# Performance work log

Hardware: AMD Instinct MI355X
Metric: run time of the kernel (lower is better)

Reference implementation:

```python
import jax, jax.numpy as jnp
import numpy as np

N, E, G = 50000, 800000, 64
IN_DIM, HID, HEADS = 8, 64, 4
HC = HID * HEADS  # 256
EPS = 1e-5


def _gatv2(h, src, dst, ea, wl, bl, wr, br, we, att, bias):
    # h: [N, F_in]; ea: [E, 1]; att: [HEADS, HID]
    xl = (h @ wl + bl).reshape(N, HEADS, HID)        # source transform
    xr = (h @ wr + br).reshape(N, HEADS, HID)        # target transform
    ee = (ea @ we).reshape(E, HEADS, HID)            # edge embedding (no bias)
    m = xl[src] + xr[dst] + ee                       # [E, H, C]
    m = jax.nn.leaky_relu(m, 0.2)
    logits = jnp.einsum('ehc,hc->eh', m, att)        # [E, H]
    # softmax over incoming edges of each target node
    mx = jax.ops.segment_max(logits, dst, num_segments=N)
    ex = jnp.exp(logits - mx[dst])
    den = jax.ops.segment_sum(ex, dst, num_segments=N)
    alpha = ex / den[dst]                            # [E, H]
    out = jax.ops.segment_sum(xl[src] * alpha[..., None], dst, num_segments=N)
    return out.reshape(N, HC) + bias


def setup_inputs() -> dict:
    key = jax.random.key(0)
    ks = jax.random.split(key, 32)
    s = lambda fan: 1.0 / np.sqrt(fan)
    d = {}
    d['x'] = jax.random.normal(ks[0], (N, IN_DIM), jnp.float32)
    d['edge_attr'] = jax.random.normal(ks[1], (E, 1), jnp.float32)
    d['edge_index'] = jax.random.randint(ks[2], (2, E), 0, N, jnp.int64)
    d['batch'] = jnp.sort(jax.random.randint(ks[3], (N,), 0, G, jnp.int64))
    d['enc_w'] = jax.random.normal(ks[4], (IN_DIM, HID), jnp.float32) * s(IN_DIM)
    d['enc_b'] = jnp.zeros((HID,), jnp.float32)
    # gat1: in = HID
    d['g1_wl'] = jax.random.normal(ks[5], (HID, HC), jnp.float32) * s(HID)
    d['g1_bl'] = jnp.zeros((HC,), jnp.float32)
    d['g1_wr'] = jax.random.normal(ks[6], (HID, HC), jnp.float32) * s(HID)
    d['g1_br'] = jnp.zeros((HC,), jnp.float32)
    d['g1_we'] = jax.random.normal(ks[7], (1, HC), jnp.float32)
    d['g1_att'] = jax.random.normal(ks[8], (HEADS, HID), jnp.float32) * s(HID)
    d['g1_bias'] = jnp.zeros((HC,), jnp.float32)
    # gat2: in = HC
    d['g2_wl'] = jax.random.normal(ks[9], (HC, HC), jnp.float32) * s(HC)
    d['g2_bl'] = jnp.zeros((HC,), jnp.float32)
    d['g2_wr'] = jax.random.normal(ks[10], (HC, HC), jnp.float32) * s(HC)
    d['g2_br'] = jnp.zeros((HC,), jnp.float32)
    d['g2_we'] = jax.random.normal(ks[11], (1, HC), jnp.float32)
    d['g2_att'] = jax.random.normal(ks[12], (HEADS, HID), jnp.float32) * s(HID)
    d['g2_bias'] = jnp.zeros((HC,), jnp.float32)
    # post MLP + head
    d['p1_w'] = jax.random.normal(ks[13], (HC, 128), jnp.float32) * s(HC)
    d['p1_b'] = jnp.zeros((128,), jnp.float32)
    d['ln_g'] = jnp.ones((128,), jnp.float32)
    d['ln_b'] = jnp.zeros((128,), jnp.float32)
    d['p2_w'] = jax.random.normal(ks[14], (128, HID), jnp.float32) * s(128)
    d['p2_b'] = jnp.zeros((HID,), jnp.float32)
    d['head_w'] = jax.random.normal(ks[15], (HID, 1), jnp.float32) * s(HID)
    d['head_b'] = jnp.zeros((1,), jnp.float32)
    return d


def reference(x, edge_attr, edge_index, batch, enc_w, enc_b,
              g1_wl, g1_bl, g1_wr, g1_br, g1_we, g1_att, g1_bias,
              g2_wl, g2_bl, g2_wr, g2_br, g2_we, g2_att, g2_bias,
              p1_w, p1_b, ln_g, ln_b, p2_w, p2_b, head_w, head_b):
    src, dst = edge_index[0], edge_index[1]
    h = jax.nn.relu(x @ enc_w + enc_b)
    h = jax.nn.relu(_gatv2(h, src, dst, edge_attr, g1_wl, g1_bl, g1_wr, g1_br, g1_we, g1_att, g1_bias))
    h = jax.nn.relu(_gatv2(h, src, dst, edge_attr, g2_wl, g2_bl, g2_wr, g2_br, g2_we, g2_att, g2_bias))
    # global mean pool over graphs
    counts = jax.ops.segment_sum(jnp.ones((N,), h.dtype), batch, num_segments=G)
    g = jax.ops.segment_sum(h, batch, num_segments=G) / jnp.maximum(counts, 1.0)[:, None]
    # post MLP: Linear -> LayerNorm -> ReLU -> (dropout=eval noop) -> Linear -> ReLU
    z = g @ p1_w + p1_b
    mu = jnp.mean(z, axis=-1, keepdims=True)
    var = jnp.var(z, axis=-1, keepdims=True)
    z = (z - mu) * jax.lax.rsqrt(var + EPS) * ln_g + ln_b
    z = jax.nn.relu(z)
    z = jax.nn.relu(z @ p2_w + p2_b)
    return (z @ head_w + head_b)[:, 0]
```

## Files before the change

### kernel.cpp

```cpp
#include <hip/hip_runtime.h>
#include <hip/hip_bf16.h>
#include <math.h>

#define N_NODES 50000
#define N_EDGES 800000
#define N_GRAPHS 64
#define HCD 256
#define HIDD 64


__global__ void zero_i32(int* __restrict__ p, int n) {
  int i = blockIdx.x * blockDim.x + threadIdx.x;
  if (i < n) p[i] = 0;
}

__global__ void hist_kernel(const int* __restrict__ dst, int* __restrict__ counts, int ne) {
  int i = blockIdx.x * blockDim.x + threadIdx.x;
  if (i < ne) atomicAdd(&counts[dst[i]], 1);
}

__global__ __launch_bounds__(256) void scan1_kernel(const int* __restrict__ counts,
                                                    int* __restrict__ offs,
                                                    int* __restrict__ bsum, int n) {
  int t = threadIdx.x, lane = t & 63, w = t >> 6;
  int i = blockIdx.x * 256 + t;
  int v = (i < n) ? counts[i] : 0;
  int x = v;
  #pragma unroll
  for (int off = 1; off < 64; off <<= 1) {
    int tmp = __shfl_up(x, off);
    if (lane >= off) x += tmp;
  }
  __shared__ int wsum[4], woff[4];
  if (lane == 63) wsum[w] = x;
  __syncthreads();
  if (t == 0) {
    int s = 0;
    #pragma unroll
    for (int k = 0; k < 4; ++k) { woff[k] = s; s += wsum[k]; }
    bsum[blockIdx.x] = s;
  }
  __syncthreads();
  if (i < n) offs[i] = woff[w] + x - v;
}

__global__ __launch_bounds__(256) void scan2_kernel(int* __restrict__ bsum, int nblk) {
  int t = threadIdx.x, lane = t & 63, w = t >> 6;
  int v = (t < nblk) ? bsum[t] : 0;
  int x = v;
  #pragma unroll
  for (int off = 1; off < 64; off <<= 1) {
    int tmp = __shfl_up(x, off);
    if (lane >= off) x += tmp;
  }
  __shared__ int wsum[4], woff[4];
  if (lane == 63) wsum[w] = x;
  __syncthreads();
  if (t == 0) {
    int s = 0;
    #pragma unroll
    for (int k = 0; k < 4; ++k) { woff[k] = s; s += wsum[k]; }
  }
  __syncthreads();
  if (t < nblk) bsum[t] = woff[w] + x - v;
}

__global__ void scan3_kernel(int* __restrict__ offs, const int* __restrict__ bsum,
                             int* __restrict__ cursor, int n) {
  int i = blockIdx.x * blockDim.x + threadIdx.x;
  if (i < n) {
    int v = offs[i] + bsum[i >> 8];
    offs[i] = v;
    cursor[i] = v;
  } else if (i == n) {
    offs[n] = N_EDGES;
  }
}

__global__ void scatter_kernel(const int* __restrict__ src, const int* __restrict__ dst,
                               const float* __restrict__ ea, int* __restrict__ cursor,
                               int* __restrict__ ssrc, float* __restrict__ sea, int ne) {
  int i = blockIdx.x * blockDim.x + threadIdx.x;
  if (i < ne) {
    int d = dst[i];
    int pos = atomicAdd(&cursor[d], 1);
    ssrc[pos] = src[i];
    sea[pos] = ea[i];
  }
}


__global__ void encoder_kernel(const float* __restrict__ x, const float* __restrict__ w,
                               const float* __restrict__ b, float* __restrict__ h0, int n_nodes) {
  int idx = blockIdx.x * blockDim.x + threadIdx.x;
  if (idx >= n_nodes * HIDD) return;
  int n = idx >> 6, c = idx & 63;
  float acc = b[c];
  #pragma unroll
  for (int k = 0; k < 8; ++k) acc += x[n * 8 + k] * w[k * 64 + c];
  h0[idx] = fmaxf(acc, 0.f);
}


template<int K>
__global__ __launch_bounds__(256) void transform_kernel(
    const float* __restrict__ h,
    const float* __restrict__ wl, const float* __restrict__ bl,
    const float* __restrict__ wr, const float* __restrict__ br,
    float* __restrict__ xl, float* __restrict__ xr, int n_nodes)
{
  constexpr int NT = 32;
  __shared__ float hs[NT * K];
  int n0 = blockIdx.x * NT;
  const float* __restrict__ w   = blockIdx.y ? wr : wl;
  const float* __restrict__ bb  = blockIdx.y ? br : bl;
  float* __restrict__ outp      = blockIdx.y ? xr : xl;

  for (int idx4 = threadIdx.x; idx4 < NT * K / 4; idx4 += 256) {
    int i = idx4 / (K / 4), kq = idx4 - i * (K / 4);
    int n = n0 + i;
    float4 v = make_float4(0.f, 0.f, 0.f, 0.f);
    if (n < n_nodes) v = *(const float4*)&h[n * K + 4 * kq];
    *(float4*)&hs[i * K + 4 * kq] = v;
  }
  __syncthreads();

  const int cx = threadIdx.x & 63;
  const int ny = threadIdx.x >> 6;
  float acc[8][4];
  #pragma unroll
  for (int i = 0; i < 8; ++i)
    #pragma unroll
    for (int j = 0; j < 4; ++j) acc[i][j] = 0.f;

  const float* hrow = &hs[(ny * 8) * K];
  float4 wc = *(const float4*)&w[4 * cx];
  for (int k = 0; k < K; ++k) {
    float4 wn = wc;
    if (k + 1 < K) wn = *(const float4*)&w[(k + 1) * 256 + 4 * cx];
    #pragma unroll
    for (int i = 0; i < 8; ++i) {
      float hv = hrow[i * K + k];
      acc[i][0] = fmaf(hv, wc.x, acc[i][0]);
      acc[i][1] = fmaf(hv, wc.y, acc[i][1]);
      acc[i][2] = fmaf(hv, wc.z, acc[i][2]);
      acc[i][3] = fmaf(hv, wc.w, acc[i][3]);
    }
    wc = wn;
  }

  float4 b4 = *(const float4*)&bb[4 * cx];
  #pragma unroll
  for (int i = 0; i < 8; ++i) {
    int n = n0 + ny * 8 + i;
    if (n < n_nodes) {
      float4 o;
      o.x = acc[i][0] + b4.x; o.y = acc[i][1] + b4.y;
      o.z = acc[i][2] + b4.z; o.w = acc[i][3] + b4.w;
      *(float4*)&outp[n * 256 + 4 * cx] = o;
    }
  }
}


__global__ __launch_bounds__(256) void gat_aggregate_kernel(
    const float* __restrict__ xl, const float* __restrict__ xr,
    const int* __restrict__ offs, const int* __restrict__ ssrc,
    const float* __restrict__ sea,
    const float* __restrict__ we, const float* __restrict__ att,
    const float* __restrict__ bias, float* __restrict__ out, int n_nodes)
{
  int n = blockIdx.x;
  if (n >= n_nodes) return;
  int t = threadIdx.x, lane = t & 63, wv = t >> 6;
  const float4 xr4 = *(const float4*)&xr[n * HCD + 4 * lane];
  const float4 we4 = *(const float4*)&we[4 * lane];
  const float4 at4 = *(const float4*)&att[4 * lane];
  int beg = offs[n], end = offs[n + 1];
  float runmax = -INFINITY, den = 0.f;
  float4 acc = make_float4(0.f, 0.f, 0.f, 0.f);

  int j = beg + wv;
  int s = (j < end) ? ssrc[j] : 0;
  float eav = (j < end) ? sea[j] : 0.f;
  while (j < end) {
    int jn = j + 4;
    int s2 = 0; float ea2 = 0.f;
    if (jn < end) { s2 = ssrc[jn]; ea2 = sea[jn]; }
    float4 xlv = *(const float4*)&xl[s * HCD + 4 * lane];
    float4 m;
    m.x = xlv.x + fmaf(eav, we4.x, xr4.x);
    m.y = xlv.y + fmaf(eav, we4.y, xr4.y);
    m.z = xlv.z + fmaf(eav, we4.z, xr4.z);
    m.w = xlv.w + fmaf(eav, we4.w, xr4.w);
    m.x = (m.x > 0.f) ? m.x : 0.2f * m.x;
    m.y = (m.y > 0.f) ? m.y : 0.2f * m.y;
    m.z = (m.z > 0.f) ? m.z : 0.2f * m.z;
    m.w = (m.w > 0.f) ? m.w : 0.2f * m.w;
    float p = fmaf(m.w, at4.w, fmaf(m.z, at4.z, fmaf(m.y, at4.y, m.x * at4.x)));
    #pragma unroll
    for (int off = 1; off < 16; off <<= 1) p += __shfl_xor(p, off);
    float nm = fmaxf(runmax, p);
    float sc = __expf(runmax - nm);
    float wgt = __expf(p - nm);
    den = fmaf(den, sc, wgt);
    acc.x = fmaf(acc.x, sc, wgt * xlv.x);
    acc.y = fmaf(acc.y, sc, wgt * xlv.y);
    acc.z = fmaf(acc.z, sc, wgt * xlv.z);
    acc.w = fmaf(acc.w, sc, wgt * xlv.w);
    runmax = nm;
    s = s2; eav = ea2; j = jn;
  }

  __shared__ float smax[4][64], sden[4][64];
  __shared__ float4 sacc[4][64];
  smax[wv][lane] = runmax; sden[wv][lane] = den; sacc[wv][lane] = acc;
  __syncthreads();
  if (wv == 0) {
    float m0 = smax[0][lane], m1 = smax[1][lane], m2 = smax[2][lane], m3 = smax[3][lane];
    float M = fmaxf(fmaxf(m0, m1), fmaxf(m2, m3));
    float4 a = make_float4(0.f, 0.f, 0.f, 0.f);
    if (M > -INFINITY) {
      float s0 = __expf(m0 - M), s1 = __expf(m1 - M), s2 = __expf(m2 - M), s3 = __expf(m3 - M);
      float d = sden[0][lane] * s0 + sden[1][lane] * s1 + sden[2][lane] * s2 + sden[3][lane] * s3;
      float4 a0 = sacc[0][lane], a1 = sacc[1][lane], a2 = sacc[2][lane], a3 = sacc[3][lane];
      a.x = a0.x * s0 + a1.x * s1 + a2.x * s2 + a3.x * s3;
      a.y = a0.y * s0 + a1.y * s1 + a2.y * s2 + a3.y * s3;
      a.z = a0.z * s0 + a1.z * s1 + a2.z * s2 + a3.z * s3;
      a.w = a0.w * s0 + a1.w * s1 + a2.w * s2 + a3.w * s3;
      float inv = 1.f / d;
      a.x *= inv; a.y *= inv; a.z *= inv; a.w *= inv;
    }
    float4 b4 = *(const float4*)&bias[4 * lane];
    float4 o;
    o.x = fmaxf(a.x + b4.x, 0.f);
    o.y = fmaxf(a.y + b4.y, 0.f);
    o.z = fmaxf(a.z + b4.z, 0.f);
    o.w = fmaxf(a.w + b4.w, 0.f);
    *(float4*)&out[n * HCD + 4 * lane] = o;
  }
}


__device__ __forceinline__ int lbound(const int* __restrict__ a, int n, int key) {
  int lo = 0, hi = n;
  while (lo < hi) { int mid = (lo + hi) >> 1; if (a[mid] < key) lo = mid + 1; else hi = mid; }
  return lo;
}

__global__ __launch_bounds__(256) void pool_kernel(const float* __restrict__ h,
                                                   const int* __restrict__ batch,
                                                   float* __restrict__ gmean) {
  int g = blockIdx.x;
  int t = threadIdx.x, lane = t & 63, wv = t >> 6;
  __shared__ int sb, se;
  if (t == 0) {
    sb = lbound(batch, N_NODES, g);
    se = lbound(batch, N_NODES, g + 1);
  }
  __syncthreads();
  int beg = sb, end = se;
  float4 acc = make_float4(0.f, 0.f, 0.f, 0.f);
  for (int n = beg + wv; n < end; n += 4) {
    float4 v = *(const float4*)&h[n * HCD + 4 * lane];
    acc.x += v.x; acc.y += v.y; acc.z += v.z; acc.w += v.w;
  }
  __shared__ float4 sacc[4][64];
  sacc[wv][lane] = acc;
  __syncthreads();
  if (wv == 0) {
    float4 a0 = sacc[0][lane], a1 = sacc[1][lane], a2 = sacc[2][lane], a3 = sacc[3][lane];
    float cnt = (float)((end - beg) > 1 ? (end - beg) : 1);
    float inv = 1.f / cnt;
    float4 o;
    o.x = (a0.x + a1.x + a2.x + a3.x) * inv;
    o.y = (a0.y + a1.y + a2.y + a3.y) * inv;
    o.z = (a0.z + a1.z + a2.z + a3.z) * inv;
    o.w = (a0.w + a1.w + a2.w + a3.w) * inv;
    *(float4*)&gmean[g * HCD + 4 * lane] = o;
  }
}


__global__ __launch_bounds__(128) void mlp_kernel(
    const float* __restrict__ gmean,
    const float* __restrict__ p1_w, const float* __restrict__ p1_b,
    const float* __restrict__ ln_g, const float* __restrict__ ln_b,
    const float* __restrict__ p2_w, const float* __restrict__ p2_b,
    const float* __restrict__ head_w, const float* __restrict__ head_b,
    float* __restrict__ out)
{
  int g = blockIdx.x, t = threadIdx.x;
  __shared__ float gv[256];
  __shared__ float zs[128];
  __shared__ float z2s[64];
  __shared__ float sums[2][2];
  gv[t] = gmean[g * 256 + t];
  gv[t + 128] = gmean[g * 256 + 128 + t];
  __syncthreads();
  float acc = p1_b[t];
  for (int k = 0; k < 256; ++k) acc += gv[k] * p1_w[k * 128 + t];
  float s1 = acc, s2 = acc * acc;
  #pragma unroll
  for (int off = 32; off >= 1; off >>= 1) {
    s1 += __shfl_xor(s1, off);
    s2 += __shfl_xor(s2, off);
  }
  int wid = t >> 6, lane = t & 63;
  if (lane == 0) { sums[wid][0] = s1; sums[wid][1] = s2; }
  __syncthreads();
  float S1 = sums[0][0] + sums[1][0];
  float S2 = sums[0][1] + sums[1][1];
  float mu = S1 * (1.f / 128.f);
  float var = S2 * (1.f / 128.f) - mu * mu;
  float rstd = rsqrtf(var + 1e-5f);
  float z = (acc - mu) * rstd * ln_g[t] + ln_b[t];
  zs[t] = fmaxf(z, 0.f);
  __syncthreads();
  if (t < 64) {
    float a2 = p2_b[t];
    for (int k = 0; k < 128; ++k) a2 += zs[k] * p2_w[k * 64 + t];
    z2s[t] = fmaxf(a2, 0.f);
  }
  __syncthreads();
  if (t < 64) {
    float p = z2s[t] * head_w[t];
    #pragma unroll
    for (int off = 32; off >= 1; off >>= 1) p += __shfl_xor(p, off);
    if (t == 0) out[g] = p + head_b[0];
  }
}


extern "C" void kernel_launch(void* const* d_in, const int* in_sizes, int n_in,
                              void* d_out, int out_size, void* d_ws, size_t ws_size,
                              hipStream_t stream) {
  const float* x       = (const float*)d_in[0];
  const float* ea      = (const float*)d_in[1];
  const int*   eidx    = (const int*)d_in[2];
  const int*   batch   = (const int*)d_in[3];
  const float* enc_w   = (const float*)d_in[4];
  const float* enc_b   = (const float*)d_in[5];
  const float* g1_wl   = (const float*)d_in[6];
  const float* g1_bl   = (const float*)d_in[7];
  const float* g1_wr   = (const float*)d_in[8];
  const float* g1_br   = (const float*)d_in[9];
  const float* g1_we   = (const float*)d_in[10];
  const float* g1_att  = (const float*)d_in[11];
  const float* g1_bias = (const float*)d_in[12];
  const float* g2_wl   = (const float*)d_in[13];
  const float* g2_bl   = (const float*)d_in[14];
  const float* g2_wr   = (const float*)d_in[15];
  const float* g2_br   = (const float*)d_in[16];
  const float* g2_we   = (const float*)d_in[17];
  const float* g2_att  = (const float*)d_in[18];
  const float* g2_bias = (const float*)d_in[19];
  const float* p1_w    = (const float*)d_in[20];
  const float* p1_b    = (const float*)d_in[21];
  const float* ln_g    = (const float*)d_in[22];
  const float* ln_b    = (const float*)d_in[23];
  const float* p2_w    = (const float*)d_in[24];
  const float* p2_b    = (const float*)d_in[25];
  const float* head_w  = (const float*)d_in[26];
  const float* head_b  = (const float*)d_in[27];

  const int* src = eidx;
  const int* dst = eidx + N_EDGES;

  char* wsp = (char*)d_ws;
  size_t off = 0;
  auto alloc = [&](size_t bytes) -> void* {
    void* p = wsp + off;
    off += (bytes + 255) & ~(size_t)255;
    return p;
  };
  float* h0     = (float*)alloc((size_t)N_NODES * 64 * 4);
  float* hA     = (float*)alloc((size_t)N_NODES * 256 * 4);
  float* xl     = (float*)alloc((size_t)N_NODES * 256 * 4);
  float* xr     = (float*)alloc((size_t)N_NODES * 256 * 4);
  int*   counts = (int*)alloc((size_t)N_NODES * 4);
  int*   offs   = (int*)alloc((size_t)(N_NODES + 1) * 4);
  int*   cursor = (int*)alloc((size_t)N_NODES * 4);
  int*   bsum   = (int*)alloc((size_t)256 * 4);
  int*   ssrc   = (int*)alloc((size_t)N_EDGES * 4);
  float* seaf   = (float*)alloc((size_t)N_EDGES * 4);
  float* gmean  = (float*)alloc((size_t)N_GRAPHS * 256 * 4);

  const int NBLK = (N_NODES + 255) / 256;

  zero_i32<<<NBLK, 256, 0, stream>>>(counts, N_NODES);
  hist_kernel<<<(N_EDGES + 255) / 256, 256, 0, stream>>>(dst, counts, N_EDGES);
  scan1_kernel<<<NBLK, 256, 0, stream>>>(counts, offs, bsum, N_NODES);
  scan2_kernel<<<1, 256, 0, stream>>>(bsum, NBLK);
  scan3_kernel<<<(N_NODES + 256) / 256, 256, 0, stream>>>(offs, bsum, cursor, N_NODES);
  scatter_kernel<<<(N_EDGES + 255) / 256, 256, 0, stream>>>(src, dst, ea, cursor, ssrc, seaf, N_EDGES);

  encoder_kernel<<<(N_NODES * 64 + 255) / 256, 256, 0, stream>>>(x, enc_w, enc_b, h0, N_NODES);

  const dim3 tgrid((N_NODES + 31) / 32, 2);

  transform_kernel<64><<<tgrid, 256, 0, stream>>>(
      h0, g1_wl, g1_bl, g1_wr, g1_br, xl, xr, N_NODES);
  gat_aggregate_kernel<<<N_NODES, 256, 0, stream>>>(
      xl, xr, offs, ssrc, seaf, g1_we, g1_att, g1_bias, hA, N_NODES);

  transform_kernel<256><<<tgrid, 256, 0, stream>>>(
      hA, g2_wl, g2_bl, g2_wr, g2_br, xl, xr, N_NODES);
  gat_aggregate_kernel<<<N_NODES, 256, 0, stream>>>(
      xl, xr, offs, ssrc, seaf, g2_we, g2_att, g2_bias, hA, N_NODES);

  pool_kernel<<<N_GRAPHS, 256, 0, stream>>>(hA, batch, gmean);
  mlp_kernel<<<N_GRAPHS, 128, 0, stream>>>(gmean, p1_w, p1_b, ln_g, ln_b,
                                           p2_w, p2_b, head_w, head_b, (float*)d_out);
}
```

Before: 755.5 us.

## Retile transform GEMM with K-tiled transposed smem and prefetch gathered xl rows

The node transform kernel now processes 64 nodes per block with 16 accumulator rows per thread, staging h in K-chunks of 64 into a transposed shared tile so each thread reads its h values as float4 vectors. This halves the number of weight reloads per node and reduces LDS instruction count, at the cost of more registers, now constrained by a launch-bounds occupancy hint. The aggregation kernel additionally prefetches the next edge's gathered xl row one iteration ahead to hide gather latency, which adds register pressure.

```diff
diff --git a/kernel.cpp b/kernel.cpp
--- a/kernel.cpp
+++ b/kernel.cpp
@@ -103,56 +103,87 @@
 
 
 template<int K>
-__global__ __launch_bounds__(256) void transform_kernel(
+__global__ __launch_bounds__(256, 4) void transform_kernel(
     const float* __restrict__ h,
     const float* __restrict__ wl, const float* __restrict__ bl,
     const float* __restrict__ wr, const float* __restrict__ br,
     float* __restrict__ xl, float* __restrict__ xr, int n_nodes)
 {
-  constexpr int NT = 32;
-  __shared__ float hs[NT * K];
-  int n0 = blockIdx.x * NT;
+  constexpr int NT = 64;
+  constexpr int KT = 64;
+  __shared__ float hs[KT][NT];
+  const int n0 = blockIdx.x * NT;
   const float* __restrict__ w   = blockIdx.y ? wr : wl;
   const float* __restrict__ bb  = blockIdx.y ? br : bl;
   float* __restrict__ outp      = blockIdx.y ? xr : xl;
 
-  for (int idx4 = threadIdx.x; idx4 < NT * K / 4; idx4 += 256) {
-    int i = idx4 / (K / 4), kq = idx4 - i * (K / 4);
-    int n = n0 + i;
-    float4 v = make_float4(0.f, 0.f, 0.f, 0.f);
-    if (n < n_nodes) v = *(const float4*)&h[n * K + 4 * kq];
-    *(float4*)&hs[i * K + 4 * kq] = v;
-  }
-  __syncthreads();
-
-  const int cx = threadIdx.x & 63;
-  const int ny = threadIdx.x >> 6;
-  float acc[8][4];
-  #pragma unroll
-  for (int i = 0; i < 8; ++i)
+  const int t  = threadIdx.x;
+  const int cx = t & 63;
+  const int g  = t >> 6;
+
+  float acc[16][4];
+  #pragma unroll
+  for (int i = 0; i < 16; ++i)
     #pragma unroll
     for (int j = 0; j < 4; ++j) acc[i][j] = 0.f;
 
-  const float* hrow = &hs[(ny * 8) * K];
   float4 wc = *(const float4*)&w[4 * cx];
-  for (int k = 0; k < K; ++k) {
-    float4 wn = wc;
-    if (k + 1 < K) wn = *(const float4*)&w[(k + 1) * 256 + 4 * cx];
-    #pragma unroll
-    for (int i = 0; i < 8; ++i) {
-      float hv = hrow[i * K + k];
-      acc[i][0] = fmaf(hv, wc.x, acc[i][0]);
-      acc[i][1] = fmaf(hv, wc.y, acc[i][1]);
-      acc[i][2] = fmaf(hv, wc.z, acc[i][2]);
-      acc[i][3] = fmaf(hv, wc.w, acc[i][3]);
+  const int sn = t & 63;
+
+  for (int kt = 0; kt < K; kt += KT) {
+    #pragma unroll
+    for (int rep = 0; rep < 4; ++rep) {
+      int kq = (t >> 6) + rep * 4;
+      float4 v = make_float4(0.f, 0.f, 0.f, 0.f);
+      if (n0 + sn < n_nodes) v = *(const float4*)&h[(n0 + sn) * K + kt + 4 * kq];
+      hs[4 * kq + 0][sn] = v.x;
+      hs[4 * kq + 1][sn] = v.y;
+      hs[4 * kq + 2][sn] = v.z;
+      hs[4 * kq + 3][sn] = v.w;
     }
-    wc = wn;
+    __syncthreads();
+
+    for (int kk = 0; kk < KT; ++kk) {
+      int k = kt + kk;
+      float4 wn = wc;
+      if (k + 1 < K) wn = *(const float4*)&w[(k + 1) * 256 + 4 * cx];
+      const float* hrow = &hs[kk][g * 16];
+      float4 hA = *(const float4*)&hrow[0];
+      float4 hB = *(const float4*)&hrow[4];
+      float4 hC = *(const float4*)&hrow[8];
+      float4 hD = *(const float4*)&hrow[12];
+      #pragma unroll
+      for (int j = 0; j < 4; ++j) {
+        float hv0 = (j == 0) ? hA.x : (j == 1) ? hA.y : (j == 2) ? hA.z : hA.w;
+        float hv1 = (j == 0) ? hB.x : (j == 1) ? hB.y : (j == 2) ? hB.z : hB.w;
+        float hv2 = (j == 0) ? hC.x : (j == 1) ? hC.y : (j == 2) ? hC.z : hC.w;
+        float hv3 = (j == 0) ? hD.x : (j == 1) ? hD.y : (j == 2) ? hD.z : hD.w;
+        acc[j][0]      = fmaf(hv0, wc.x, acc[j][0]);
+        acc[j][1]      = fmaf(hv0, wc.y, acc[j][1]);
+        acc[j][2]      = fmaf(hv0, wc.z, acc[j][2]);
+        acc[j][3]      = fmaf(hv0, wc.w, acc[j][3]);
+        acc[j + 4][0]  = fmaf(hv1, wc.x, acc[j + 4][0]);
+        acc[j + 4][1]  = fmaf(hv1, wc.y, acc[j + 4][1]);
+        acc[j + 4][2]  = fmaf(hv1, wc.z, acc[j + 4][2]);
+        acc[j + 4][3]  = fmaf(hv1, wc.w, acc[j + 4][3]);
+        acc[j + 8][0]  = fmaf(hv2, wc.x, acc[j + 8][0]);
+        acc[j + 8][1]  = fmaf(hv2, wc.y, acc[j + 8][1]);
+        acc[j + 8][2]  = fmaf(hv2, wc.z, acc[j + 8][2]);
+        acc[j + 8][3]  = fmaf(hv2, wc.w, acc[j + 8][3]);
+        acc[j + 12][0] = fmaf(hv3, wc.x, acc[j + 12][0]);
+        acc[j + 12][1] = fmaf(hv3, wc.y, acc[j + 12][1]);
+        acc[j + 12][2] = fmaf(hv3, wc.z, acc[j + 12][2]);
+        acc[j + 12][3] = fmaf(hv3, wc.w, acc[j + 12][3]);
+      }
+      wc = wn;
+    }
+    __syncthreads();
   }
 
   float4 b4 = *(const float4*)&bb[4 * cx];
   #pragma unroll
-  for (int i = 0; i < 8; ++i) {
-    int n = n0 + ny * 8 + i;
+  for (int i = 0; i < 16; ++i) {
+    int n = n0 + g * 16 + i;
     if (n < n_nodes) {
       float4 o;
       o.x = acc[i][0] + b4.x; o.y = acc[i][1] + b4.y;
@@ -181,13 +212,22 @@
   float4 acc = make_float4(0.f, 0.f, 0.f, 0.f);
 
   int j = beg + wv;
-  int s = (j < end) ? ssrc[j] : 0;
-  float eav = (j < end) ? sea[j] : 0.f;
+  float eav = 0.f;
+  float4 xlv = make_float4(0.f, 0.f, 0.f, 0.f);
+  if (j < end) {
+    int s = ssrc[j];
+    eav = sea[j];
+    xlv = *(const float4*)&xl[s * HCD + 4 * lane];
+  }
   while (j < end) {
     int jn = j + 4;
-    int s2 = 0; float ea2 = 0.f;
-    if (jn < end) { s2 = ssrc[jn]; ea2 = sea[jn]; }
-    float4 xlv = *(const float4*)&xl[s * HCD + 4 * lane];
+    float ea2 = 0.f;
+    float4 xlv2 = make_float4(0.f, 0.f, 0.f, 0.f);
+    if (jn < end) {
+      int s2 = ssrc[jn];
+      ea2 = sea[jn];
+      xlv2 = *(const float4*)&xl[s2 * HCD + 4 * lane];
+    }
     float4 m;
     m.x = xlv.x + fmaf(eav, we4.x, xr4.x);
     m.y = xlv.y + fmaf(eav, we4.y, xr4.y);
@@ -209,7 +249,7 @@
     acc.z = fmaf(acc.z, sc, wgt * xlv.z);
     acc.w = fmaf(acc.w, sc, wgt * xlv.w);
     runmax = nm;
-    s = s2; eav = ea2; j = jn;
+    xlv = xlv2; eav = ea2; j = jn;
   }
 
   __shared__ float smax[4][64], sden[4][64];
@@ -397,7 +437,7 @@
 
   encoder_kernel<<<(N_NODES * 64 + 255) / 256, 256, 0, stream>>>(x, enc_w, enc_b, h0, N_NODES);
 
-  const dim3 tgrid((N_NODES + 31) / 32, 2);
+  const dim3 tgrid((N_NODES + 63) / 64, 2);
 
   transform_kernel<64><<<tgrid, 256, 0, stream>>>(
       h0, g1_wl, g1_bl, g1_wr, g1_br, xl, xr, N_NODES);
```

Measured after the change: 925.1 us. +22.4%, slower.

## Assign one wavefront per node in GAT aggregation, dropping cross-wave LDS merge

Applied to the files above, without the earlier changes.

The aggregation kernel now maps each 64-lane wavefront to its own destination node, so a block handles four nodes instead of one. This removes the shared-memory merge of partial softmax states and the block barrier. The edge loop is now serial per node, and the next source row's xl vector is prefetched one edge ahead to hide gather latency. The trade-off is less memory-level parallelism per node, with one gather in flight per wave instead of four, and nodes of uneven degree now sit together in the same block.

```diff
diff --git a/kernel.cpp b/kernel.cpp
--- a/kernel.cpp
+++ b/kernel.cpp
@@ -170,9 +170,9 @@
     const float* __restrict__ we, const float* __restrict__ att,
     const float* __restrict__ bias, float* __restrict__ out, int n_nodes)
 {
-  int n = blockIdx.x;
+  int n = blockIdx.x * 4 + (threadIdx.x >> 6);
   if (n >= n_nodes) return;
-  int t = threadIdx.x, lane = t & 63, wv = t >> 6;
+  int lane = threadIdx.x & 63;
   const float4 xr4 = *(const float4*)&xr[n * HCD + 4 * lane];
   const float4 we4 = *(const float4*)&we[4 * lane];
   const float4 at4 = *(const float4*)&att[4 * lane];
@@ -180,14 +180,23 @@
   float runmax = -INFINITY, den = 0.f;
   float4 acc = make_float4(0.f, 0.f, 0.f, 0.f);
 
-  int j = beg + wv;
-  int s = (j < end) ? ssrc[j] : 0;
-  float eav = (j < end) ? sea[j] : 0.f;
+  int j = beg;
+  float eav = 0.f;
+  float4 xlv = make_float4(0.f, 0.f, 0.f, 0.f);
+  if (j < end) {
+    int s = ssrc[j];
+    eav = sea[j];
+    xlv = *(const float4*)&xl[s * HCD + 4 * lane];
+  }
   while (j < end) {
-    int jn = j + 4;
-    int s2 = 0; float ea2 = 0.f;
-    if (jn < end) { s2 = ssrc[jn]; ea2 = sea[jn]; }
-    float4 xlv = *(const float4*)&xl[s * HCD + 4 * lane];
+    int jn = j + 1;
+    float ea2 = 0.f;
+    float4 xlv2 = make_float4(0.f, 0.f, 0.f, 0.f);
+    if (jn < end) {
+      int s2 = ssrc[jn];
+      ea2 = sea[jn];
+      xlv2 = *(const float4*)&xl[s2 * HCD + 4 * lane];
+    }
     float4 m;
     m.x = xlv.x + fmaf(eav, we4.x, xr4.x);
     m.y = xlv.y + fmaf(eav, we4.y, xr4.y);
@@ -209,36 +218,17 @@
     acc.z = fmaf(acc.z, sc, wgt * xlv.z);
     acc.w = fmaf(acc.w, sc, wgt * xlv.w);
     runmax = nm;
-    s = s2; eav = ea2; j = jn;
-  }
-
-  __shared__ float smax[4][64], sden[4][64];
-  __shared__ float4 sacc[4][64];
-  smax[wv][lane] = runmax; sden[wv][lane] = den; sacc[wv][lane] = acc;
-  __syncthreads();
-  if (wv == 0) {
-    float m0 = smax[0][lane], m1 = smax[1][lane], m2 = smax[2][lane], m3 = smax[3][lane];
-    float M = fmaxf(fmaxf(m0, m1), fmaxf(m2, m3));
-    float4 a = make_float4(0.f, 0.f, 0.f, 0.f);
-    if (M > -INFINITY) {
-      float s0 = __expf(m0 - M), s1 = __expf(m1 - M), s2 = __expf(m2 - M), s3 = __expf(m3 - M);
-      float d = sden[0][lane] * s0 + sden[1][lane] * s1 + sden[2][lane] * s2 + sden[3][lane] * s3;
-      float4 a0 = sacc[0][lane], a1 = sacc[1][lane], a2 = sacc[2][lane], a3 = sacc[3][lane];
-      a.x = a0.x * s0 + a1.x * s1 + a2.x * s2 + a3.x * s3;
-      a.y = a0.y * s0 + a1.y * s1 + a2.y * s2 + a3.y * s3;
-      a.z = a0.z * s0 + a1.z * s1 + a2.z * s2 + a3.z * s3;
-      a.w = a0.w * s0 + a1.w * s1 + a2.w * s2 + a3.w * s3;
-      float inv = 1.f / d;
-      a.x *= inv; a.y *= inv; a.z *= inv; a.w *= inv;
-    }
-    float4 b4 = *(const float4*)&bias[4 * lane];
-    float4 o;
-    o.x = fmaxf(a.x + b4.x, 0.f);
-    o.y = fmaxf(a.y + b4.y, 0.f);
-    o.z = fmaxf(a.z + b4.z, 0.f);
-    o.w = fmaxf(a.w + b4.w, 0.f);
-    *(float4*)&out[n * HCD + 4 * lane] = o;
-  }
+    xlv = xlv2; eav = ea2; j = jn;
+  }
+
+  float inv = (end > beg) ? (1.f / den) : 0.f;
+  float4 b4 = *(const float4*)&bias[4 * lane];
+  float4 o;
+  o.x = fmaxf(fmaf(acc.x, inv, b4.x), 0.f);
+  o.y = fmaxf(fmaf(acc.y, inv, b4.y), 0.f);
+  o.z = fmaxf(fmaf(acc.z, inv, b4.z), 0.f);
+  o.w = fmaxf(fmaf(acc.w, inv, b4.w), 0.f);
+  *(float4*)&out[n * HCD + 4 * lane] = o;
 }
 
 
@@ -398,15 +388,16 @@
   encoder_kernel<<<(N_NODES * 64 + 255) / 256, 256, 0, stream>>>(x, enc_w, enc_b, h0, N_NODES);
 
   const dim3 tgrid((N_NODES + 31) / 32, 2);
+  const int AGG_BLOCKS = (N_NODES + 3) / 4;
 
   transform_kernel<64><<<tgrid, 256, 0, stream>>>(
       h0, g1_wl, g1_bl, g1_wr, g1_br, xl, xr, N_NODES);
-  gat_aggregate_kernel<<<N_NODES, 256, 0, stream>>>(
+  gat_aggregate_kernel<<<AGG_BLOCKS, 256, 0, stream>>>(
       xl, xr, offs, ssrc, seaf, g1_we, g1_att, g1_bias, hA, N_NODES);
 
   transform_kernel<256><<<tgrid, 256, 0, stream>>>(
       hA, g2_wl, g2_bl, g2_wr, g2_br, xl, xr, N_NODES);
-  gat_aggregate_kernel<<<N_NODES, 256, 0, stream>>>(
+  gat_aggregate_kernel<<<AGG_BLOCKS, 256, 0, stream>>>(
       xl, xr, offs, ssrc, seaf, g2_we, g2_att, g2_bias, hA, N_NODES);
 
   pool_kernel<<<N_GRAPHS, 256, 0, stream>>>(hA, batch, gmean);
```

After: 766.9 us. No clear change (+1.5%).
